# Kernel optimization log

Measured on AMD Instinct MI355X. Metric: run time of the kernel, lower is better.

## Reference

```python
import jax, jax.numpy as jnp
import numpy as np

B, N, E, H, D, F = 2, 4096, 128, 8, 16, 512
EPS = 1e-6


def _rms_norm(x, w):
    xf = x.astype(jnp.float32)
    n = xf * jax.lax.rsqrt(jnp.mean(xf * xf, axis=-1, keepdims=True) + EPS)
    return n.astype(x.dtype) * w


def setup_inputs() -> dict:
    key = jax.random.key(0)
    ks = jax.random.split(key, 12)
    s = 1.0 / np.sqrt(E)
    sf = 1.0 / np.sqrt(F)
    coords = jax.random.uniform(ks[10], (B, N, 2))
    dis = jnp.sqrt(jnp.sum((coords[:, :, None, :] - coords[:, None, :, :]) ** 2, -1))
    dis = dis * (1.0 - jnp.eye(N))  # zero diagonal
    return {
        "input1": jax.random.normal(ks[0], (B, N, E), jnp.float32),
        "dis_matrix": dis.astype(jnp.float32),
        "Wq": jax.random.uniform(ks[1], (E, E), jnp.float32, -s, s),
        "Wk": jax.random.uniform(ks[2], (E, E), jnp.float32, -s, s),
        "Wv": jax.random.uniform(ks[3], (E, E), jnp.float32, -s, s),
        "alpha": jnp.float32(1.0),
        "ln1_w": jnp.ones((E,), jnp.float32),
        "ln2_w": jnp.ones((E,), jnp.float32),
        "Wcomb": jax.random.uniform(ks[4], (E, E), jnp.float32, -s, s),
        "W1": jax.random.uniform(ks[5], (F, E), jnp.float32, -s, s),
        "b1": jax.random.uniform(ks[6], (F,), jnp.float32, -s, s),
        "W2": jax.random.uniform(ks[7], (E, F), jnp.float32, -sf, sf),
        "b2": jax.random.uniform(ks[8], (E,), jnp.float32, -sf, sf),
    }


def _sparse_attention_afm(x, dis_matrix, Wq, Wk, Wv, alpha):
    # project and split heads: [B,N,E] -> [B,H,N,D]
    def heads(w):
        return (x @ w.T).reshape(B, N, H, D).transpose(0, 2, 1, 3)
    q, k, v = heads(Wq), heads(Wk), heads(Wv)
    log2n = jnp.float32(np.log2(N))
    dis_weight = jnp.exp(-alpha * log2n * dis_matrix)  # [B,N,N] (i,j)
    k_weight = jnp.exp(k)  # [B,H,N,D]
    w1 = jnp.einsum('bij,bhik->bhjk', dis_weight, k_weight * v)
    w2 = jnp.einsum('bij,bhik->bhjk', dis_weight, k_weight)
    out = jax.nn.sigmoid(q) * (w1 / w2)  # [B,H,N,D]
    return out.transpose(0, 2, 1, 3).reshape(B, N, E)


def reference(input1, dis_matrix, Wq, Wk, Wv, alpha, ln1_w, ln2_w, Wcomb, W1, b1, W2, b2):
    h = _rms_norm(input1, ln1_w)
    attn = _sparse_attention_afm(h, dis_matrix, Wq, Wk, Wv, alpha)
    out1 = input1 + attn @ Wcomb.T
    h2 = _rms_norm(out1, ln2_w)
    ffn = jax.nn.relu(h2 @ W1.T + b1) @ W2.T + b2
    return out1 + ffn
```

## Files before the change

kernel.cpp:

```cpp
#include <hip/hip_runtime.h>

#define NTOK 4096
#define EDIM 128

typedef __attribute__((ext_vector_type(8))) short bf16x8;
typedef __attribute__((ext_vector_type(4))) float f32x4;

__device__ __forceinline__ ushort f2bf(float x) {
    union { float f; unsigned u; } c; c.f = x;
    unsigned r = c.u + 0x7FFF + ((c.u >> 16) & 1);
    return (ushort)(r >> 16);
}

__device__ __forceinline__ int swz64(int r, int k)  { return r * 64  + (k ^ ((r & 7) << 3)); }
__device__ __forceinline__ int swz128(int r, int k) { return r * 128 + (k ^ ((r & 7) << 3)); }

__device__ __forceinline__ void stage_w(const float* __restrict__ W, ushort* Bs) {
    const int t = threadIdx.x;
    const int br = t >> 1, h = (t & 1) * 64;
    const float* src = W + (size_t)br * 128 + h;
    ushort* dst = Bs + br * 136 + h;
#pragma unroll
    for (int j = 0; j < 8; ++j) {
        float4 u = *(const float4*)(src + j * 8);
        float4 v = *(const float4*)(src + j * 8 + 4);
        bf16x8 o;
        o[0] = (short)f2bf(u.x); o[1] = (short)f2bf(u.y);
        o[2] = (short)f2bf(u.z); o[3] = (short)f2bf(u.w);
        o[4] = (short)f2bf(v.x); o[5] = (short)f2bf(v.y);
        o[6] = (short)f2bf(v.z); o[7] = (short)f2bf(v.w);
        *(bf16x8*)(dst + j * 8) = o;
    }
}

__device__ __forceinline__ void gemm128(const ushort* __restrict__ As,
                                        const ushort* __restrict__ Bs,
                                        f32x4 (&acc)[2][2], int lane, int wv) {
    const int m15 = lane & 15, kq = (lane >> 4) * 8, c0w = wv * 32;
#pragma unroll
    for (int kc = 0; kc < 4; ++kc) {
        int ko = kc * 32 + kq;
        bf16x8 a0 = *(const bf16x8*)&As[m15 * 136 + ko];
        bf16x8 a1 = *(const bf16x8*)&As[(16 + m15) * 136 + ko];
        bf16x8 b0 = *(const bf16x8*)&Bs[(c0w + m15) * 136 + ko];
        bf16x8 b1 = *(const bf16x8*)&Bs[(c0w + 16 + m15) * 136 + ko];
        acc[0][0] = __builtin_amdgcn_mfma_f32_16x16x32_bf16(a0, b0, acc[0][0], 0, 0, 0);
        acc[0][1] = __builtin_amdgcn_mfma_f32_16x16x32_bf16(a0, b1, acc[0][1], 0, 0, 0);
        acc[1][0] = __builtin_amdgcn_mfma_f32_16x16x32_bf16(a1, b0, acc[1][0], 0, 0, 0);
        acc[1][1] = __builtin_amdgcn_mfma_f32_16x16x32_bf16(a1, b1, acc[1][1], 0, 0, 0);
    }
}

__device__ __forceinline__ void gemm_dirB(const ushort* __restrict__ As,
                                          const ushort* __restrict__ W, int ldb,
                                          f32x4 (&acc)[2][2], int lane, int wv) {
    const int m15 = lane & 15, kq = (lane >> 4) * 8, c0w = wv * 32;
#pragma unroll
    for (int kc = 0; kc < 4; ++kc) {
        int ko = kc * 32 + kq;
        bf16x8 a0 = *(const bf16x8*)&As[swz128(m15, ko)];
        bf16x8 a1 = *(const bf16x8*)&As[swz128(16 + m15, ko)];
        bf16x8 b0 = *(const bf16x8*)&W[(size_t)(c0w + m15) * ldb + ko];
        bf16x8 b1 = *(const bf16x8*)&W[(size_t)(c0w + 16 + m15) * ldb + ko];
        acc[0][0] = __builtin_amdgcn_mfma_f32_16x16x32_bf16(a0, b0, acc[0][0], 0, 0, 0);
        acc[0][1] = __builtin_amdgcn_mfma_f32_16x16x32_bf16(a0, b1, acc[0][1], 0, 0, 0);
        acc[1][0] = __builtin_amdgcn_mfma_f32_16x16x32_bf16(a1, b0, acc[1][0], 0, 0, 0);
        acc[1][1] = __builtin_amdgcn_mfma_f32_16x16x32_bf16(a1, b1, acc[1][1], 0, 0, 0);
    }
}

__launch_bounds__(256, 2)
__global__ void qkv_k(const float* __restrict__ input1, const float* __restrict__ ln1w,
                      const float* __restrict__ Wq, const float* __restrict__ Wk,
                      const float* __restrict__ Wv,
                      const float* __restrict__ Wc, const float* __restrict__ W1,
                      const float* __restrict__ W2, ushort* __restrict__ Wbf,
                      float* __restrict__ sigq, ushort* __restrict__ Mt) {
    const int bx = blockIdx.x;
    if (bx >= 256) {
        int g = ((bx - 256) * 256 + threadIdx.x) * 4;
        const float* src; ushort* dst;
        if (g < 16384)      { src = Wc + g;           dst = Wbf + 49152 + g; }
        else if (g < 81920) { src = W1 + (g - 16384); dst = Wbf + 65536 + (g - 16384); }
        else                { src = W2 + (g - 81920); dst = Wbf + 131072 + (g - 81920); }
        float4 u = *(const float4*)src;
        ushort4 o; o.x = f2bf(u.x); o.y = f2bf(u.y); o.z = f2bf(u.z); o.w = f2bf(u.w);
        *(ushort4*)dst = o;
        return;
    }
    __shared__ ushort As[32 * 136];
    __shared__ ushort Bs0[128 * 136];
    __shared__ ushort Bs1[128 * 136];
    const int t = threadIdx.x, lane = t & 63, wv = t >> 6;
    const int m15 = lane & 15, quad = lane >> 4, c0w = wv * 32;
    const int M0 = bx * 32;

    {
        const int row = t >> 3, seg = t & 7;
        const float* xp = input1 + (size_t)(M0 + row) * 128 + seg * 16;
        float4 x[4]; float ss = 0.f;
#pragma unroll
        for (int i = 0; i < 4; ++i) {
            x[i] = *(const float4*)(xp + i * 4);
            ss += x[i].x * x[i].x + x[i].y * x[i].y + x[i].z * x[i].z + x[i].w * x[i].w;
        }
        ss += __shfl_down(ss, 4, 8);
        ss += __shfl_down(ss, 2, 8);
        ss += __shfl_down(ss, 1, 8);
        ss = __shfl(ss, 0, 8);
        float rr = rsqrtf(ss * (1.0f / 128.0f) + 1e-6f);
#pragma unroll
        for (int i = 0; i < 4; ++i) {
            float4 w4 = *(const float4*)&ln1w[seg * 16 + i * 4];
            ushort4 o;
            o.x = f2bf(x[i].x * rr * w4.x);
            o.y = f2bf(x[i].y * rr * w4.y);
            o.z = f2bf(x[i].z * rr * w4.z);
            o.w = f2bf(x[i].w * rr * w4.w);
            *(ushort4*)&As[row * 136 + seg * 16 + i * 4] = o;
        }
    }
    stage_w(Wq, Bs0);
    __syncthreads();
    {
        f32x4 acc[2][2] = {};
        gemm128(As, Bs0, acc, lane, wv);
        stage_w(Wk, Bs1);
#pragma unroll
        for (int mi = 0; mi < 2; ++mi)
#pragma unroll
            for (int ni = 0; ni < 2; ++ni)
#pragma unroll
                for (int r = 0; r < 4; ++r) {
                    int row = M0 + mi * 16 + quad * 4 + r;
                    int lc  = c0w + ni * 16 + m15;
                    sigq[(size_t)row * 128 + lc] = 1.0f / (1.0f + __expf(-acc[mi][ni][r]));
                }
    }
    __syncthreads();
    f32x4 acck[2][2] = {};
    gemm128(As, Bs1, acck, lane, wv);
    stage_w(Wv, Bs0);
    __syncthreads();
    f32x4 accv[2][2] = {};
    gemm128(As, Bs0, accv, lane, wv);
    const int b = M0 >> 12, i0 = M0 & (NTOK - 1);
#pragma unroll
    for (int mi = 0; mi < 2; ++mi)
#pragma unroll
        for (int ni = 0; ni < 2; ++ni) {
            int e = c0w + ni * 16 + m15;
            ushort* mt0 = Mt + ((size_t)b * 256 + e) * NTOK;
            ushort* mt1 = mt0 + (size_t)128 * NTOK;
            int ib = i0 + mi * 16 + quad * 4;
            ushort4 pv, pk;
            float kw0 = __expf(acck[mi][ni][0]); pv.x = f2bf(kw0 * accv[mi][ni][0]); pk.x = f2bf(kw0);
            float kw1 = __expf(acck[mi][ni][1]); pv.y = f2bf(kw1 * accv[mi][ni][1]); pk.y = f2bf(kw1);
            float kw2 = __expf(acck[mi][ni][2]); pv.z = f2bf(kw2 * accv[mi][ni][2]); pk.z = f2bf(kw2);
            float kw3 = __expf(acck[mi][ni][3]); pv.w = f2bf(kw3 * accv[mi][ni][3]); pk.w = f2bf(kw3);
            *(ushort4*)&mt0[ib] = pv;
            *(ushort4*)&mt1[ib] = pk;
        }
}

__launch_bounds__(512, 2)
__global__ void big_gemm_k(const float* __restrict__ dis, const float* __restrict__ alphap,
                           const ushort* __restrict__ Mt, float* __restrict__ P) {
    __shared__ ushort As[32 * 64];
    const int t = threadIdx.x, lane = t & 63, wv = t >> 6;
    const int m15 = lane & 15, quad = lane >> 4, kq = quad * 8;
    const int b  = blockIdx.x & 1;
    const int j0 = (blockIdx.x >> 1) * 32;
    const float coef = -alphap[0] * 12.0f;
    const ushort* Mtb = Mt + (size_t)b * 256 * NTOK;
    float* outp = P + (size_t)b * NTOK * 256;

    const int sr = t >> 4, sk = (t & 15) * 4;
    const float* arow = dis + (size_t)b * NTOK * NTOK + (size_t)(j0 + sr) * NTOK + sk;
    const int c0 = wv * 32;

    f32x4 acc[2][2] = {};
    float4 fa_e, fa_o;
    bf16x8 pb[2][2], pbn[2][2];
    fa_e = *(const float4*)(arow);
    fa_o = *(const float4*)(arow + 64);
#pragma unroll
    for (int kh = 0; kh < 2; ++kh)
#pragma unroll
        for (int ni = 0; ni < 2; ++ni)
            pb[kh][ni] = *(const bf16x8*)&Mtb[(size_t)(c0 + ni * 16 + m15) * NTOK + kh * 32 + kq];

#define BIG_ITER(FA, PBC, PBN, IT) do {                                         \
    ushort4 a4;                                                                 \
    a4.x = f2bf(__expf(coef * FA.x));                                           \
    a4.y = f2bf(__expf(coef * FA.y));                                           \
    a4.z = f2bf(__expf(coef * FA.z));                                           \
    a4.w = f2bf(__expf(coef * FA.w));                                           \
    *(ushort4*)&As[swz64(sr, sk)] = a4;                                         \
    __syncthreads();                                                            \
    {   int itA = (IT) + 2;                                                     \
        if (itA < 64) FA = *(const float4*)(arow + itA * 64);                   \
        int itB = (IT) + 1; int kb_ = (itB < 64) ? itB * 64 : 0;                \
        _Pragma("unroll") for (int kh = 0; kh < 2; ++kh)                        \
        _Pragma("unroll") for (int ni = 0; ni < 2; ++ni)                        \
            PBN[kh][ni] = *(const bf16x8*)&Mtb[(size_t)(c0 + ni * 16 + m15) * NTOK + kb_ + kh * 32 + kq]; } \
    _Pragma("unroll") for (int kh = 0; kh < 2; ++kh) {                          \
        bf16x8 a0 = *(const bf16x8*)&As[swz64(m15, kh * 32 + kq)];              \
        bf16x8 a1 = *(const bf16x8*)&As[swz64(16 + m15, kh * 32 + kq)];         \
        acc[0][0] = __builtin_amdgcn_mfma_f32_16x16x32_bf16(a0, PBC[kh][0], acc[0][0], 0, 0, 0); \
        acc[0][1] = __builtin_amdgcn_mfma_f32_16x16x32_bf16(a0, PBC[kh][1], acc[0][1], 0, 0, 0); \
        acc[1][0] = __builtin_amdgcn_mfma_f32_16x16x32_bf16(a1, PBC[kh][0], acc[1][0], 0, 0, 0); \
        acc[1][1] = __builtin_amdgcn_mfma_f32_16x16x32_bf16(a1, PBC[kh][1], acc[1][1], 0, 0, 0); \
    }                                                                           \
    __syncthreads();                                                            \
} while (0)

    for (int it2 = 0; it2 < 32; ++it2) {
        BIG_ITER(fa_e, pb, pbn, it2 * 2);
        BIG_ITER(fa_o, pbn, pb, it2 * 2 + 1);
    }
#undef BIG_ITER

#pragma unroll
    for (int mi = 0; mi < 2; ++mi)
#pragma unroll
        for (int ni = 0; ni < 2; ++ni)
#pragma unroll
            for (int r = 0; r < 4; ++r) {
                int j = j0 + mi * 16 + quad * 4 + r;
                int c = c0 + ni * 16 + m15;
                outp[(size_t)j * 256 + c] = acc[mi][ni][r];
            }
}

__launch_bounds__(256, 1)
__global__ void tail_k(const float* __restrict__ sigq, const float* __restrict__ P,
                       const ushort* __restrict__ Wbf,
                       const float* __restrict__ input1, const float* __restrict__ b1,
                       const float* __restrict__ b2, const float* __restrict__ ln2w,
                       float* __restrict__ out) {
    __shared__ ushort As[32 * 128];
    __shared__ ushort As2[32 * 128];
    __shared__ float  O[32][132];
    const int t = threadIdx.x, lane = t & 63, wv = t >> 6;
    const int m15 = lane & 15, quad = lane >> 4, c0w = wv * 32;
    const int M0 = blockIdx.x * 32;

    {
        const int ar = t >> 3, e0 = (t & 7) * 16;
        const int g = M0 + ar;
        const float4* sg = (const float4*)(sigq + (size_t)g * 128 + e0);
        const float4* pu = (const float4*)(P + (size_t)g * 256 + e0);
        const float4* pd = (const float4*)(P + (size_t)g * 256 + 128 + e0);
#pragma unroll
        for (int i = 0; i < 4; ++i) {
            float4 s = sg[i], u = pu[i], d = pd[i];
            ushort4 a;
            a.x = f2bf(s.x * u.x / d.x);
            a.y = f2bf(s.y * u.y / d.y);
            a.z = f2bf(s.z * u.z / d.z);
            a.w = f2bf(s.w * u.w / d.w);
            *(ushort4*)&As[swz128(ar, e0 + i * 4)] = a;
        }
    }
    __syncthreads();
    f32x4 acc[2][2] = {};
    gemm_dirB(As, Wbf + 49152, 128, acc, lane, wv);
#pragma unroll
    for (int mi = 0; mi < 2; ++mi)
#pragma unroll
        for (int ni = 0; ni < 2; ++ni)
#pragma unroll
            for (int r = 0; r < 4; ++r) {
                int rl  = mi * 16 + quad * 4 + r;
                int col = c0w + ni * 16 + m15;
                O[rl][col] = acc[mi][ni][r] + input1[(size_t)(M0 + rl) * 128 + col];
            }
    __syncthreads();
    {
        const int row = t >> 3, seg = t & 7;
        float4 x[4]; float ss = 0.f;
#pragma unroll
        for (int i = 0; i < 4; ++i) {
            x[i] = *(const float4*)&O[row][seg * 16 + i * 4];
            ss += x[i].x * x[i].x + x[i].y * x[i].y + x[i].z * x[i].z + x[i].w * x[i].w;
        }
        ss += __shfl_down(ss, 4, 8);
        ss += __shfl_down(ss, 2, 8);
        ss += __shfl_down(ss, 1, 8);
        ss = __shfl(ss, 0, 8);
        float rr = rsqrtf(ss * (1.0f / 128.0f) + 1e-6f);
#pragma unroll
        for (int i = 0; i < 4; ++i) {
            float4 w4 = *(const float4*)&ln2w[seg * 16 + i * 4];
            ushort4 o;
            o.x = f2bf(x[i].x * rr * w4.x);
            o.y = f2bf(x[i].y * rr * w4.y);
            o.z = f2bf(x[i].z * rr * w4.z);
            o.w = f2bf(x[i].w * rr * w4.w);
            *(ushort4*)&As[swz128(row, seg * 16 + i * 4)] = o;
        }
    }
    f32x4 aout[2][2] = {};
    for (int f0 = 0; f0 < 4; ++f0) {
        __syncthreads();
        f32x4 am[2][2] = {};
        gemm_dirB(As, Wbf + 65536 + f0 * 128 * 128, 128, am, lane, wv);
#pragma unroll
        for (int mi = 0; mi < 2; ++mi)
#pragma unroll
            for (int ni = 0; ni < 2; ++ni)
#pragma unroll
                for (int r = 0; r < 4; ++r) {
                    int rl  = mi * 16 + quad * 4 + r;
                    int col = c0w + ni * 16 + m15;
                    As2[swz128(rl, col)] = f2bf(fmaxf(am[mi][ni][r] + b1[f0 * 128 + col], 0.0f));
                }
        __syncthreads();
        gemm_dirB(As2, Wbf + 131072 + f0 * 128, 512, aout, lane, wv);
    }
#pragma unroll
    for (int mi = 0; mi < 2; ++mi)
#pragma unroll
        for (int ni = 0; ni < 2; ++ni)
#pragma unroll
            for (int r = 0; r < 4; ++r) {
                int rl  = mi * 16 + quad * 4 + r;
                int col = c0w + ni * 16 + m15;
                out[(size_t)(M0 + rl) * 128 + col] = (O[rl][col] + b2[col]) + aout[mi][ni][r];
            }
}

extern "C" void kernel_launch(void* const* d_in, const int* in_sizes, int n_in,
                              void* d_out, int out_size, void* d_ws, size_t ws_size,
                              hipStream_t stream) {
    const float* input1 = (const float*)d_in[0];
    const float* dis    = (const float*)d_in[1];
    const float* Wq     = (const float*)d_in[2];
    const float* Wk     = (const float*)d_in[3];
    const float* Wv     = (const float*)d_in[4];
    const float* alpha  = (const float*)d_in[5];
    const float* ln1    = (const float*)d_in[6];
    const float* ln2    = (const float*)d_in[7];
    const float* Wcomb  = (const float*)d_in[8];
    const float* W1     = (const float*)d_in[9];
    const float* b1     = (const float*)d_in[10];
    const float* W2     = (const float*)d_in[11];
    const float* b2     = (const float*)d_in[12];
    float* out = (float*)d_out;

    char* w8 = (char*)d_ws;
    ushort* Wbf  = (ushort*)(w8);
    float*  sigq = (float*)(w8 + (4u << 20));
    ushort* Mt   = (ushort*)(w8 + (8u << 20));
    float*  P    = (float*)(w8 + (12u << 20));

    qkv_k<<<dim3(400), 256, 0, stream>>>(input1, ln1, Wq, Wk, Wv,
                                         Wcomb, W1, W2, Wbf, sigq, Mt);
    big_gemm_k<<<dim3(256), 512, 0, stream>>>(dis, alpha, Mt, P);
    tail_k<<<dim3(256), 256, 0, stream>>>(sigq, P, Wbf, input1, b1, b2, ln2, out);
}
```

Baseline: 286.7 us.

## Split-K the distance GEMM with larger row tiles and double-buffered LDS

The distance-weighted GEMM now splits the K (token) dimension in two halves, writing partial sums to two buffers that the tail kernel adds before dividing. Each block covers 64 output rows instead of 32, so every B fragment loaded from Mt feeds twice as many MFMAs. The A tile is double-buffered in LDS so one barrier per iteration is enough, and exp is computed with exp2f on a prescaled coefficient. The cost is extra P traffic for two partial buffers, more accumulator registers, and hand-placed scheduling barriers.

Result: faster. 258.3 us (-9.9%).

```diff
diff --git a/kernel.cpp b/kernel.cpp
--- a/kernel.cpp
+++ b/kernel.cpp
@@ -165,64 +165,103 @@
 
 __launch_bounds__(512, 2)
 __global__ void big_gemm_k(const float* __restrict__ dis, const float* __restrict__ alphap,
-                           const ushort* __restrict__ Mt, float* __restrict__ P) {
-    __shared__ ushort As[32 * 64];
+                           const ushort* __restrict__ Mt,
+                           float* __restrict__ P0, float* __restrict__ P1) {
+    __shared__ ushort As[2][64 * 64];
     const int t = threadIdx.x, lane = t & 63, wv = t >> 6;
     const int m15 = lane & 15, quad = lane >> 4, kq = quad * 8;
     const int b  = blockIdx.x & 1;
-    const int j0 = (blockIdx.x >> 1) * 32;
-    const float coef = -alphap[0] * 12.0f;
+    const int s  = (blockIdx.x >> 1) & 1;
+    const int j0 = (blockIdx.x >> 2) * 64;
+    const float coefl2 = -alphap[0] * 12.0f * 1.44269504088896f;
+    const float* disb = dis + (size_t)b * NTOK * NTOK;
     const ushort* Mtb = Mt + (size_t)b * 256 * NTOK;
-    float* outp = P + (size_t)b * NTOK * 256;
-
-    const int sr = t >> 4, sk = (t & 15) * 4;
-    const float* arow = dis + (size_t)b * NTOK * NTOK + (size_t)(j0 + sr) * NTOK + sk;
+    float* outp = ((s == 0) ? P0 : P1) + (size_t)b * NTOK * 256;
+    const int k0 = s * (NTOK / 2);
+
+    const int sr = t >> 3, sk = (t & 7) * 8;
+    const float* arow = disb + (size_t)(j0 + sr) * NTOK + k0 + sk;
     const int c0 = wv * 32;
-
-    f32x4 acc[2][2] = {};
-    float4 fa_e, fa_o;
+    const ushort* Bp = Mtb + (size_t)(c0 + m15) * NTOK + k0 + kq;
+    const ushort* Bp1 = Bp + (size_t)16 * NTOK;
+
+    f32x4 acc[4][2] = {};
+    float4 fa0, fa1, fb0, fb1;
     bf16x8 pb[2][2], pbn[2][2];
-    fa_e = *(const float4*)(arow);
-    fa_o = *(const float4*)(arow + 64);
-#pragma unroll
-    for (int kh = 0; kh < 2; ++kh)
-#pragma unroll
-        for (int ni = 0; ni < 2; ++ni)
-            pb[kh][ni] = *(const bf16x8*)&Mtb[(size_t)(c0 + ni * 16 + m15) * NTOK + kh * 32 + kq];
-
-#define BIG_ITER(FA, PBC, PBN, IT) do {                                         \
-    ushort4 a4;                                                                 \
-    a4.x = f2bf(__expf(coef * FA.x));                                           \
-    a4.y = f2bf(__expf(coef * FA.y));                                           \
-    a4.z = f2bf(__expf(coef * FA.z));                                           \
-    a4.w = f2bf(__expf(coef * FA.w));                                           \
-    *(ushort4*)&As[swz64(sr, sk)] = a4;                                         \
-    __syncthreads();                                                            \
-    {   int itA = (IT) + 2;                                                     \
-        if (itA < 64) FA = *(const float4*)(arow + itA * 64);                   \
-        int itB = (IT) + 1; int kb_ = (itB < 64) ? itB * 64 : 0;                \
-        _Pragma("unroll") for (int kh = 0; kh < 2; ++kh)                        \
-        _Pragma("unroll") for (int ni = 0; ni < 2; ++ni)                        \
-            PBN[kh][ni] = *(const bf16x8*)&Mtb[(size_t)(c0 + ni * 16 + m15) * NTOK + kb_ + kh * 32 + kq]; } \
+
+    {
+        float4 g0 = *(const float4*)(arow);
+        float4 g1 = *(const float4*)(arow + 4);
+        bf16x8 a8;
+        a8[0] = (short)f2bf(exp2f(coefl2 * g0.x));
+        a8[1] = (short)f2bf(exp2f(coefl2 * g0.y));
+        a8[2] = (short)f2bf(exp2f(coefl2 * g0.z));
+        a8[3] = (short)f2bf(exp2f(coefl2 * g0.w));
+        a8[4] = (short)f2bf(exp2f(coefl2 * g1.x));
+        a8[5] = (short)f2bf(exp2f(coefl2 * g1.y));
+        a8[6] = (short)f2bf(exp2f(coefl2 * g1.z));
+        a8[7] = (short)f2bf(exp2f(coefl2 * g1.w));
+        *(bf16x8*)&As[0][swz64(sr, sk)] = a8;
+        fa0 = *(const float4*)(arow + 64);
+        fa1 = *(const float4*)(arow + 68);
+#pragma unroll
+        for (int kh = 0; kh < 2; ++kh) {
+            pb[kh][0] = *(const bf16x8*)&Bp[kh * 32];
+            pb[kh][1] = *(const bf16x8*)&Bp1[kh * 32];
+        }
+        __syncthreads();
+    }
+
+#define BIG_ITER(FAc0, FAc1, FAn0, FAn1, PBC, PBN, BUFC, BUFN, IT) do {         \
+    {   int ia = (IT) + 2; int ka = (ia < 32) ? ia * 64 : 0;                    \
+        FAn0 = *(const float4*)(arow + ka);                                     \
+        FAn1 = *(const float4*)(arow + ka + 4);                                 \
+        int ib = (IT) + 1; int kb_ = (ib < 32) ? ib * 64 : 0;                   \
+        _Pragma("unroll") for (int kh = 0; kh < 2; ++kh) {                      \
+            PBN[kh][0] = *(const bf16x8*)&Bp[kb_ + kh * 32];                    \
+            PBN[kh][1] = *(const bf16x8*)&Bp1[kb_ + kh * 32];                   \
+        } }                                                                     \
+    __builtin_amdgcn_sched_barrier(0);                                          \
+    {   bf16x8 a8;                                                              \
+        a8[0] = (short)f2bf(exp2f(coefl2 * FAc0.x));                            \
+        a8[1] = (short)f2bf(exp2f(coefl2 * FAc0.y));                            \
+        a8[2] = (short)f2bf(exp2f(coefl2 * FAc0.z));                            \
+        a8[3] = (short)f2bf(exp2f(coefl2 * FAc0.w));                            \
+        a8[4] = (short)f2bf(exp2f(coefl2 * FAc1.x));                            \
+        a8[5] = (short)f2bf(exp2f(coefl2 * FAc1.y));                            \
+        a8[6] = (short)f2bf(exp2f(coefl2 * FAc1.z));                            \
+        a8[7] = (short)f2bf(exp2f(coefl2 * FAc1.w));                            \
+        *(bf16x8*)&BUFN[swz64(sr, sk)] = a8; }                                  \
     _Pragma("unroll") for (int kh = 0; kh < 2; ++kh) {                          \
-        bf16x8 a0 = *(const bf16x8*)&As[swz64(m15, kh * 32 + kq)];              \
-        bf16x8 a1 = *(const bf16x8*)&As[swz64(16 + m15, kh * 32 + kq)];         \
+        bf16x8 a0 = *(const bf16x8*)&BUFC[swz64(m15,      kh * 32 + kq)];       \
+        bf16x8 a1 = *(const bf16x8*)&BUFC[swz64(16 + m15, kh * 32 + kq)];       \
+        bf16x8 a2 = *(const bf16x8*)&BUFC[swz64(32 + m15, kh * 32 + kq)];       \
+        bf16x8 a3 = *(const bf16x8*)&BUFC[swz64(48 + m15, kh * 32 + kq)];       \
         acc[0][0] = __builtin_amdgcn_mfma_f32_16x16x32_bf16(a0, PBC[kh][0], acc[0][0], 0, 0, 0); \
         acc[0][1] = __builtin_amdgcn_mfma_f32_16x16x32_bf16(a0, PBC[kh][1], acc[0][1], 0, 0, 0); \
         acc[1][0] = __builtin_amdgcn_mfma_f32_16x16x32_bf16(a1, PBC[kh][0], acc[1][0], 0, 0, 0); \
         acc[1][1] = __builtin_amdgcn_mfma_f32_16x16x32_bf16(a1, PBC[kh][1], acc[1][1], 0, 0, 0); \
+        acc[2][0] = __builtin_amdgcn_mfma_f32_16x16x32_bf16(a2, PBC[kh][0], acc[2][0], 0, 0, 0); \
+        acc[2][1] = __builtin_amdgcn_mfma_f32_16x16x32_bf16(a2, PBC[kh][1], acc[2][1], 0, 0, 0); \
+        acc[3][0] = __builtin_amdgcn_mfma_f32_16x16x32_bf16(a3, PBC[kh][0], acc[3][0], 0, 0, 0); \
+        acc[3][1] = __builtin_amdgcn_mfma_f32_16x16x32_bf16(a3, PBC[kh][1], acc[3][1], 0, 0, 0); \
     }                                                                           \
-    __syncthreads();                                                            \
+    __builtin_amdgcn_sched_barrier(0);                                          \
+    asm volatile("s_waitcnt lgkmcnt(0)" ::: "memory");                          \
+    __builtin_amdgcn_s_barrier();                                               \
+    __builtin_amdgcn_sched_barrier(0);                                          \
 } while (0)
 
-    for (int it2 = 0; it2 < 32; ++it2) {
-        BIG_ITER(fa_e, pb, pbn, it2 * 2);
-        BIG_ITER(fa_o, pbn, pb, it2 * 2 + 1);
+#pragma unroll 1
+    for (int u = 0; u < 16; ++u) {
+        int IT = u * 2;
+        BIG_ITER(fa0, fa1, fb0, fb1, pb, pbn, As[0], As[1], IT);
+        BIG_ITER(fb0, fb1, fa0, fa1, pbn, pb, As[1], As[0], IT + 1);
     }
 #undef BIG_ITER
 
 #pragma unroll
-    for (int mi = 0; mi < 2; ++mi)
+    for (int mi = 0; mi < 4; ++mi)
 #pragma unroll
         for (int ni = 0; ni < 2; ++ni)
 #pragma unroll
@@ -234,7 +273,8 @@
 }
 
 __launch_bounds__(256, 1)
-__global__ void tail_k(const float* __restrict__ sigq, const float* __restrict__ P,
+__global__ void tail_k(const float* __restrict__ sigq,
+                       const float* __restrict__ P0, const float* __restrict__ P1,
                        const ushort* __restrict__ Wbf,
                        const float* __restrict__ input1, const float* __restrict__ b1,
                        const float* __restrict__ b2, const float* __restrict__ ln2w,
@@ -249,17 +289,20 @@
     {
         const int ar = t >> 3, e0 = (t & 7) * 16;
         const int g = M0 + ar;
-        const float4* sg = (const float4*)(sigq + (size_t)g * 128 + e0);
-        const float4* pu = (const float4*)(P + (size_t)g * 256 + e0);
-        const float4* pd = (const float4*)(P + (size_t)g * 256 + 128 + e0);
+        const float4* sg  = (const float4*)(sigq + (size_t)g * 128 + e0);
+        const float4* p0a = (const float4*)(P0 + (size_t)g * 256 + e0);
+        const float4* p1a = (const float4*)(P1 + (size_t)g * 256 + e0);
+        const float4* p0b = (const float4*)(P0 + (size_t)g * 256 + 128 + e0);
+        const float4* p1b = (const float4*)(P1 + (size_t)g * 256 + 128 + e0);
 #pragma unroll
         for (int i = 0; i < 4; ++i) {
-            float4 s = sg[i], u = pu[i], d = pd[i];
+            float4 s = sg[i];
+            float4 u0 = p0a[i], u1 = p1a[i], d0 = p0b[i], d1 = p1b[i];
             ushort4 a;
-            a.x = f2bf(s.x * u.x / d.x);
-            a.y = f2bf(s.y * u.y / d.y);
-            a.z = f2bf(s.z * u.z / d.z);
-            a.w = f2bf(s.w * u.w / d.w);
+            a.x = f2bf(s.x * (u0.x + u1.x) / (d0.x + d1.x));
+            a.y = f2bf(s.y * (u0.y + u1.y) / (d0.y + d1.y));
+            a.z = f2bf(s.z * (u0.z + u1.z) / (d0.z + d1.z));
+            a.w = f2bf(s.w * (u0.w + u1.w) / (d0.w + d1.w));
             *(ushort4*)&As[swz128(ar, e0 + i * 4)] = a;
         }
     }
@@ -353,10 +396,12 @@
     ushort* Wbf  = (ushort*)(w8);
     float*  sigq = (float*)(w8 + (4u << 20));
     ushort* Mt   = (ushort*)(w8 + (8u << 20));
-    float*  P    = (float*)(w8 + (12u << 20));
+    float*  P0   = (float*)(w8 + (12u << 20));
+    float*  P1   = (float*)(w8 + (20u << 20));
 
     qkv_k<<<dim3(400), 256, 0, stream>>>(input1, ln1, Wq, Wk, Wv,
                                          Wcomb, W1, W2, Wbf, sigq, Mt);
-    big_gemm_k<<<dim3(256), 512, 0, stream>>>(dis, alpha, Mt, P);
-    tail_k<<<dim3(256), 256, 0, stream>>>(sigq, P, Wbf, input1, b1, b2, ln2, out);
-}
+    big_gemm_k<<<dim3(256), 512, 0, stream>>>(dis, alpha, Mt, P0, P1);
+    tail_k<<<dim3(256), 256, 0, stream>>>(sigq, P0, P1, Wbf, input1, b1, b2,
+                                          ln2, out);
+}
```
